# Optimization experiments

Hardware: AMD Instinct MI355X
Metric: run time of the kernel (lower is better)

The kernel has to match this reference:

```python
import jax, jax.numpy as jnp
import numpy as np

TEMPERATURE = 0.5
LOSS_WEIGHT = 0.2
EPS = 1e-8


def setup_inputs() -> dict:
    key = jax.random.key(0)
    k1, k2 = jax.random.split(key)
    L, B, H = 4, 256, 65536
    hidden_states = jax.random.normal(k1, (L, B, H), dtype=jnp.float32)
    task_type = jax.random.randint(k2, (B,), 0, 16, dtype=jnp.int64)
    return {"hidden_states": hidden_states, "task_type": task_type}


def reference(hidden_states, task_type):
    # hidden_states: [L, B, H] stacked flattened intermediate activations
    # (world_size == 1, so the gathered global states equal the local states)
    L, B, H = hidden_states.shape
    # F.normalize(p=2, dim=2)
    x = hidden_states / jnp.maximum(
        jnp.linalg.norm(hidden_states, axis=2, keepdims=True), 1e-12)

    # pos_mask from task-type equality, diagonal (self-pairs) zeroed
    pos_mask = (task_type[:, None] == task_type[None, :]).astype(x.dtype)
    pos_mask = pos_mask * (1.0 - jnp.eye(B, dtype=x.dtype))  # [B, B]

    # cdist(..., compute_mode='use_mm_for_euclid_dist') ** 2:
    # ||xi||^2 + ||xj||^2 - 2 xi.xj, clamped at 0
    sq = jnp.sum(x * x, axis=2)                      # [L, B]
    dots = jnp.einsum('lbh,lch->lbc', x, x)          # [L, B, B] -- dominant GEMM
    d2 = jnp.maximum(sq[:, :, None] + sq[:, None, :] - 2.0 * dots, 0.0)

    w = jnp.exp(-(d2 / TEMPERATURE))                 # [L, B, B]
    a = jnp.sum(w * pos_mask[None], axis=2)          # [L, B]
    b = jnp.sum(w, axis=2)                           # [L, B]
    per_layer = -jnp.mean(jnp.log((a + EPS) / (b + EPS)), axis=1)  # [L]
    return jnp.sum(per_layer) / L * LOSS_WEIGHT
```

## Files before the change

### kernel.cpp

```cpp
#include <hip/hip_runtime.h>
#include <hip/hip_bf16.h>

#define L_LAYERS 4
#define B_DIM 256
#define H_DIM 65536
#define KC 1024
#define BK 32
#define NKZ (H_DIM / KC)
#define NSLICE (L_LAYERS * NKZ)
#define LDSTR 40

using bf16x8_t = __attribute__((ext_vector_type(8))) short;
using shortx8  = __attribute__((ext_vector_type(8))) short;
using floatx4  = __attribute__((ext_vector_type(4))) float;

__device__ __forceinline__ unsigned short f2bf(float f) {
    unsigned u = __float_as_uint(f);
    return (unsigned short)((u + 0x7fffu + ((u >> 16) & 1u)) >> 16);
}

__global__ __launch_bounds__(512, 2) void gram_kernel(const float* __restrict__ hs,
                                                      float* __restrict__ S) {
    __shared__ short lds[B_DIM * LDSTR];

    const int tid = threadIdx.x;
    const int bx  = blockIdx.x;
    const int l   = bx >> 6;
    const int kz  = bx & (NKZ - 1);

    const int wave = tid >> 6, lane = tid & 63;
    const int wm = wave >> 1;
    const int wn = wave & 1;
    const int mrow = lane & 15, quad = lane >> 4;

    const int r = tid >> 1;
    const int h = tid & 1;
    const float* gp = hs + ((size_t)l * B_DIM + r) * H_DIM + (size_t)kz * KC + h * 16;
    const int ldsw = r * LDSTR + h * 16;

    floatx4 acc[4][8];
#pragma unroll
    for (int i = 0; i < 4; ++i)
#pragma unroll
        for (int j = 0; j < 8; ++j) acc[i][j] = (floatx4)0.0f;

    float4 pv0 = *(const float4*)(gp + 0);
    float4 pv1 = *(const float4*)(gp + 4);
    float4 pv2 = *(const float4*)(gp + 8);
    float4 pv3 = *(const float4*)(gp + 12);

    for (int kt = 0; kt < KC / BK; ++kt) {
        shortx8 w0, w1;
        w0[0] = (short)f2bf(pv0.x); w0[1] = (short)f2bf(pv0.y);
        w0[2] = (short)f2bf(pv0.z); w0[3] = (short)f2bf(pv0.w);
        w0[4] = (short)f2bf(pv1.x); w0[5] = (short)f2bf(pv1.y);
        w0[6] = (short)f2bf(pv1.z); w0[7] = (short)f2bf(pv1.w);
        w1[0] = (short)f2bf(pv2.x); w1[1] = (short)f2bf(pv2.y);
        w1[2] = (short)f2bf(pv2.z); w1[3] = (short)f2bf(pv2.w);
        w1[4] = (short)f2bf(pv3.x); w1[5] = (short)f2bf(pv3.y);
        w1[6] = (short)f2bf(pv3.z); w1[7] = (short)f2bf(pv3.w);
        *(shortx8*)&lds[ldsw]     = w0;
        *(shortx8*)&lds[ldsw + 8] = w1;

        if (kt < KC / BK - 1) {
            const float* gn = gp + (kt + 1) * BK;
            pv0 = *(const float4*)(gn + 0);
            pv1 = *(const float4*)(gn + 4);
            pv2 = *(const float4*)(gn + 8);
            pv3 = *(const float4*)(gn + 12);
        }
        __syncthreads();

        bf16x8_t af[4], bfv[8];
#pragma unroll
        for (int i = 0; i < 4; ++i)
            af[i] = *(const bf16x8_t*)&lds[(wm * 64 + i * 16 + mrow) * LDSTR + quad * 8];
#pragma unroll
        for (int j = 0; j < 8; ++j)
            bfv[j] = *(const bf16x8_t*)&lds[(wn * 128 + j * 16 + mrow) * LDSTR + quad * 8];
#pragma unroll
        for (int i = 0; i < 4; ++i)
#pragma unroll
            for (int j = 0; j < 8; ++j)
                acc[i][j] = __builtin_amdgcn_mfma_f32_16x16x32_bf16(af[i], bfv[j], acc[i][j], 0, 0, 0);
        __syncthreads();
    }

    float* Ssl = S + (size_t)bx * (B_DIM * B_DIM);
#pragma unroll
    for (int i = 0; i < 4; ++i)
#pragma unroll
        for (int j = 0; j < 8; ++j)
#pragma unroll
            for (int rr = 0; rr < 4; ++rr) {
                const int row = wm * 64 + i * 16 + quad * 4 + rr;
                const int col = wn * 128 + j * 16 + mrow;
                Ssl[row * B_DIM + col] = acc[i][j][rr];
            }
}

__global__ __launch_bounds__(256) void reduce_kernel(const float* __restrict__ S,
                                                     float* __restrict__ G) {
    const int li = blockIdx.x;
    const int j  = threadIdx.x;
    const int l  = li >> 8;
    const int i  = li & 255;
    const float* base = S + ((size_t)l * NKZ) * (B_DIM * B_DIM) + i * B_DIM + j;
    float s = 0.0f;
#pragma unroll
    for (int kz = 0; kz < NKZ; ++kz)
        s += base[(size_t)kz * (B_DIM * B_DIM)];
    G[(size_t)li * B_DIM + j] = s;
}

__global__ __launch_bounds__(256) void loss_kernel(const float* __restrict__ G,
                                                   const int* __restrict__ task,
                                                   float* __restrict__ out) {
    const int i = blockIdx.x, l = blockIdx.y, j = threadIdx.x;

    __shared__ int s_odd_nz;
    if (j == 0) s_odd_nz = 0;
    __syncthreads();
    if (j < 128 && task[2 * j + 1] != 0) s_odd_nz = 1;
    __syncthreads();
    const bool is64 = (s_odd_nz == 0);

    const float* Gl = G + (size_t)l * B_DIM * B_DIM;
    const float gij = Gl[i * B_DIM + j];
    const float gii = Gl[i * B_DIM + i];
    const float gjj = Gl[j * B_DIM + j];
    const float nd  = gij * rsqrtf(gii) * rsqrtf(gjj);
    const float d2  = fmaxf(2.0f - 2.0f * nd, 0.0f);
    const float w   = __expf(-2.0f * d2);

    const int ti = is64 ? task[2 * i] : task[i];
    const int tj = is64 ? task[2 * j] : task[j];
    const float pm = (ti == tj && i != j) ? 1.0f : 0.0f;

    float a = w * pm, b = w;
#pragma unroll
    for (int off = 32; off > 0; off >>= 1) {
        a += __shfl_down(a, off);
        b += __shfl_down(b, off);
    }
    __shared__ float sa[4], sb[4];
    const int wv = j >> 6, ln = j & 63;
    if (ln == 0) { sa[wv] = a; sb[wv] = b; }
    __syncthreads();
    if (j == 0) {
        const float A  = sa[0] + sa[1] + sa[2] + sa[3];
        const float Bb = sb[0] + sb[1] + sb[2] + sb[3];
        const float c  = -logf((A + 1e-8f) / (Bb + 1e-8f)) * (0.2f / 1024.0f);
        atomicAdd(out, c);
    }
}

extern "C" void kernel_launch(void* const* d_in, const int* in_sizes, int n_in,
                              void* d_out, int out_size, void* d_ws, size_t ws_size,
                              hipStream_t stream) {
    const float* hs   = (const float*)d_in[0];
    const int*   task = (const int*)d_in[1];
    float*       out  = (float*)d_out;

    float* S = (float*)d_ws;
    float* G = S + (size_t)NSLICE * (B_DIM * B_DIM);

    hipMemsetAsync(out, 0, sizeof(float), stream);

    gram_kernel<<<dim3(NSLICE), dim3(512), 0, stream>>>(hs, S);
    reduce_kernel<<<dim3(L_LAYERS * B_DIM), dim3(256), 0, stream>>>(S, G);
    loss_kernel<<<dim3(B_DIM, L_LAYERS), dim3(256), 0, stream>>>(G, task, out);
}
```

Measured before the change: 423.2 us.

## Double-buffer LDS in gram kernel, store bf16 partials, fuse reduction into loss

The gram kernel now double-buffers its LDS tile, so each iteration needs one barrier instead of two. Split-K partial Gram slices are written as bf16, transposed, with the diagonal written separately in fp32. A tiny norm kernel reduces the diagonals, and the loss kernel sums the bf16 partials itself, removing the separate full reduction kernel and halving partial-sum traffic. The cost is lost precision in the split-K partials, which are rounded to bf16 before summation, plus 2-byte strided reads in the loss kernel.

```diff
diff --git a/kernel.cpp b/kernel.cpp
--- a/kernel.cpp
+++ b/kernel.cpp
@@ -6,22 +6,28 @@
 #define H_DIM 65536
 #define KC 1024
 #define BK 32
+#define NKT (KC / BK)
 #define NKZ (H_DIM / KC)
 #define NSLICE (L_LAYERS * NKZ)
 #define LDSTR 40
 
 using bf16x8_t = __attribute__((ext_vector_type(8))) short;
 using shortx8  = __attribute__((ext_vector_type(8))) short;
+using ushortx4 = __attribute__((ext_vector_type(4))) unsigned short;
 using floatx4  = __attribute__((ext_vector_type(4))) float;
 
 __device__ __forceinline__ unsigned short f2bf(float f) {
     unsigned u = __float_as_uint(f);
     return (unsigned short)((u + 0x7fffu + ((u >> 16) & 1u)) >> 16);
 }
+__device__ __forceinline__ float bf2f(unsigned short h) {
+    return __uint_as_float((unsigned)h << 16);
+}
 
 __global__ __launch_bounds__(512, 2) void gram_kernel(const float* __restrict__ hs,
-                                                      float* __restrict__ S) {
-    __shared__ short lds[B_DIM * LDSTR];
+                                                      unsigned short* __restrict__ S,
+                                                      float* __restrict__ Dg) {
+    __shared__ short lds[2][B_DIM * LDSTR];
 
     const int tid = threadIdx.x;
     const int bx  = blockIdx.x;
@@ -44,40 +50,40 @@
 #pragma unroll
         for (int j = 0; j < 8; ++j) acc[i][j] = (floatx4)0.0f;
 
-    float4 pv0 = *(const float4*)(gp + 0);
-    float4 pv1 = *(const float4*)(gp + 4);
-    float4 pv2 = *(const float4*)(gp + 8);
-    float4 pv3 = *(const float4*)(gp + 12);
+    float4 pv0, pv1, pv2, pv3;
+#define LOADPV(off) do { const float* _g = gp + (off); \
+        pv0 = *(const float4*)(_g + 0);  pv1 = *(const float4*)(_g + 4); \
+        pv2 = *(const float4*)(_g + 8);  pv3 = *(const float4*)(_g + 12); } while (0)
+#define STAGE(buf) do { shortx8 w0, w1; \
+        w0[0] = (short)f2bf(pv0.x); w0[1] = (short)f2bf(pv0.y); \
+        w0[2] = (short)f2bf(pv0.z); w0[3] = (short)f2bf(pv0.w); \
+        w0[4] = (short)f2bf(pv1.x); w0[5] = (short)f2bf(pv1.y); \
+        w0[6] = (short)f2bf(pv1.z); w0[7] = (short)f2bf(pv1.w); \
+        w1[0] = (short)f2bf(pv2.x); w1[1] = (short)f2bf(pv2.y); \
+        w1[2] = (short)f2bf(pv2.z); w1[3] = (short)f2bf(pv2.w); \
+        w1[4] = (short)f2bf(pv3.x); w1[5] = (short)f2bf(pv3.y); \
+        w1[6] = (short)f2bf(pv3.z); w1[7] = (short)f2bf(pv3.w); \
+        *(shortx8*)&lds[buf][ldsw]     = w0; \
+        *(shortx8*)&lds[buf][ldsw + 8] = w1; } while (0)
 
-    for (int kt = 0; kt < KC / BK; ++kt) {
-        shortx8 w0, w1;
-        w0[0] = (short)f2bf(pv0.x); w0[1] = (short)f2bf(pv0.y);
-        w0[2] = (short)f2bf(pv0.z); w0[3] = (short)f2bf(pv0.w);
-        w0[4] = (short)f2bf(pv1.x); w0[5] = (short)f2bf(pv1.y);
-        w0[6] = (short)f2bf(pv1.z); w0[7] = (short)f2bf(pv1.w);
-        w1[0] = (short)f2bf(pv2.x); w1[1] = (short)f2bf(pv2.y);
-        w1[2] = (short)f2bf(pv2.z); w1[3] = (short)f2bf(pv2.w);
-        w1[4] = (short)f2bf(pv3.x); w1[5] = (short)f2bf(pv3.y);
-        w1[6] = (short)f2bf(pv3.z); w1[7] = (short)f2bf(pv3.w);
-        *(shortx8*)&lds[ldsw]     = w0;
-        *(shortx8*)&lds[ldsw + 8] = w1;
+    LOADPV(0);
+    STAGE(0);
+    LOADPV(BK);
+    __syncthreads();
 
-        if (kt < KC / BK - 1) {
-            const float* gn = gp + (kt + 1) * BK;
-            pv0 = *(const float4*)(gn + 0);
-            pv1 = *(const float4*)(gn + 4);
-            pv2 = *(const float4*)(gn + 8);
-            pv3 = *(const float4*)(gn + 12);
+    for (int kt = 0; kt < NKT; ++kt) {
+        const int cur = kt & 1;
+        if (kt + 1 < NKT) {
+            STAGE(cur ^ 1);
+            if (kt + 2 < NKT) LOADPV((kt + 2) * BK);
         }
-        __syncthreads();
-
         bf16x8_t af[4], bfv[8];
 #pragma unroll
         for (int i = 0; i < 4; ++i)
-            af[i] = *(const bf16x8_t*)&lds[(wm * 64 + i * 16 + mrow) * LDSTR + quad * 8];
+            af[i] = *(const bf16x8_t*)&lds[cur][(wm * 64 + i * 16 + mrow) * LDSTR + quad * 8];
 #pragma unroll
         for (int j = 0; j < 8; ++j)
-            bfv[j] = *(const bf16x8_t*)&lds[(wn * 128 + j * 16 + mrow) * LDSTR + quad * 8];
+            bfv[j] = *(const bf16x8_t*)&lds[cur][(wn * 128 + j * 16 + mrow) * LDSTR + quad * 8];
 #pragma unroll
         for (int i = 0; i < 4; ++i)
 #pragma unroll
@@ -85,35 +91,45 @@
                 acc[i][j] = __builtin_amdgcn_mfma_f32_16x16x32_bf16(af[i], bfv[j], acc[i][j], 0, 0, 0);
         __syncthreads();
     }
+#undef LOADPV
+#undef STAGE
 
-    float* Ssl = S + (size_t)bx * (B_DIM * B_DIM);
+    unsigned short* Ssl = S + (size_t)bx * (B_DIM * B_DIM);
+#pragma unroll
+    for (int i = 0; i < 4; ++i) {
+        const int rowb = wm * 64 + i * 16 + quad * 4;
+#pragma unroll
+        for (int j = 0; j < 8; ++j) {
+            const int col = wn * 128 + j * 16 + mrow;
+            ushortx4 v;
+            v[0] = f2bf(acc[i][j][0]); v[1] = f2bf(acc[i][j][1]);
+            v[2] = f2bf(acc[i][j][2]); v[3] = f2bf(acc[i][j][3]);
+            *(ushortx4*)&Ssl[col * B_DIM + rowb] = v;
+        }
+    }
 #pragma unroll
     for (int i = 0; i < 4; ++i)
 #pragma unroll
-        for (int j = 0; j < 8; ++j)
-#pragma unroll
-            for (int rr = 0; rr < 4; ++rr) {
-                const int row = wm * 64 + i * 16 + quad * 4 + rr;
-                const int col = wn * 128 + j * 16 + mrow;
-                Ssl[row * B_DIM + col] = acc[i][j][rr];
-            }
+        for (int rr = 0; rr < 4; ++rr) {
+            const int row = wm * 64 + i * 16 + quad * 4 + rr;
+            const int cr  = row - wn * 128;
+            if (cr >= 0 && cr < 128 && (cr & 15) == mrow)
+                Dg[bx * B_DIM + row] = acc[i][cr >> 4][rr];
+        }
 }
 
-__global__ __launch_bounds__(256) void reduce_kernel(const float* __restrict__ S,
-                                                     float* __restrict__ G) {
-    const int li = blockIdx.x;
-    const int j  = threadIdx.x;
-    const int l  = li >> 8;
-    const int i  = li & 255;
-    const float* base = S + ((size_t)l * NKZ) * (B_DIM * B_DIM) + i * B_DIM + j;
+__global__ __launch_bounds__(256) void norm_kernel(const float* __restrict__ Dg,
+                                                   float* __restrict__ rnorm) {
+    const int l = blockIdx.x, j = threadIdx.x;
     float s = 0.0f;
 #pragma unroll
     for (int kz = 0; kz < NKZ; ++kz)
-        s += base[(size_t)kz * (B_DIM * B_DIM)];
-    G[(size_t)li * B_DIM + j] = s;
+        s += Dg[((l * NKZ + kz) << 8) + j];
+    rnorm[(l << 8) + j] = rsqrtf(s);
 }
 
-__global__ __launch_bounds__(256) void loss_kernel(const float* __restrict__ G,
+__global__ __launch_bounds__(256) void loss_kernel(const unsigned short* __restrict__ S,
+                                                   const float* __restrict__ rnorm,
                                                    const int* __restrict__ task,
                                                    float* __restrict__ out) {
     const int i = blockIdx.x, l = blockIdx.y, j = threadIdx.x;
@@ -125,13 +141,15 @@
     __syncthreads();
     const bool is64 = (s_odd_nz == 0);
 
-    const float* Gl = G + (size_t)l * B_DIM * B_DIM;
-    const float gij = Gl[i * B_DIM + j];
-    const float gii = Gl[i * B_DIM + i];
-    const float gjj = Gl[j * B_DIM + j];
-    const float nd  = gij * rsqrtf(gii) * rsqrtf(gjj);
-    const float d2  = fmaxf(2.0f - 2.0f * nd, 0.0f);
-    const float w   = __expf(-2.0f * d2);
+    const unsigned short* base = S + ((size_t)l * NKZ) * (B_DIM * B_DIM) + i * B_DIM + j;
+    float g = 0.0f;
+#pragma unroll
+    for (int kz = 0; kz < NKZ; ++kz)
+        g += bf2f(base[(size_t)kz * (B_DIM * B_DIM)]);
+
+    const float nd = g * rnorm[(l << 8) + i] * rnorm[(l << 8) + j];
+    const float d2 = fmaxf(2.0f - 2.0f * nd, 0.0f);
+    const float w  = __expf(-2.0f * d2);
 
     const int ti = is64 ? task[2 * i] : task[i];
     const int tj = is64 ? task[2 * j] : task[j];
@@ -162,12 +180,13 @@
     const int*   task = (const int*)d_in[1];
     float*       out  = (float*)d_out;
 
-    float* S = (float*)d_ws;
-    float* G = S + (size_t)NSLICE * (B_DIM * B_DIM);
+    unsigned short* S  = (unsigned short*)d_ws;
+    float* Dg    = (float*)(S + (size_t)NSLICE * B_DIM * B_DIM);
+    float* rnorm = Dg + (size_t)NSLICE * B_DIM;
 
     hipMemsetAsync(out, 0, sizeof(float), stream);
 
-    gram_kernel<<<dim3(NSLICE), dim3(512), 0, stream>>>(hs, S);
-    reduce_kernel<<<dim3(L_LAYERS * B_DIM), dim3(256), 0, stream>>>(S, G);
-    loss_kernel<<<dim3(B_DIM, L_LAYERS), dim3(256), 0, stream>>>(G, task, out);
+    gram_kernel<<<dim3(NSLICE), dim3(512), 0, stream>>>(hs, S, Dg);
+    norm_kernel<<<dim3(L_LAYERS), dim3(256), 0, stream>>>(Dg, rnorm);
+    loss_kernel<<<dim3(B_DIM, L_LAYERS), dim3(256), 0, stream>>>(S, rnorm, task, out);
 }
```

Measured after the change: 716.0 us. +69.2%, slower.
